# Optimization experiments

Measured on AMD Instinct MI355X. Metric: run time of the kernel, lower is better.

The kernel has to match this reference:

```python
import jax, jax.numpy as jnp
import numpy as np
from jax import lax


def T_grid(t, num_coeff):
    # Chebyshev polynomials T_0..T_{N-1} evaluated at t -> (N, len(t))
    rows = [jnp.ones_like(t), t]
    for _ in range(2, num_coeff):
        rows.append(2.0 * t * rows[-1] - rows[-2])
    return jnp.stack(rows[:num_coeff], axis=0)


def setup_inputs() -> dict:
    key = jax.random.key(0)
    k1, k2, k3, k4, k5 = jax.random.split(key, 5)
    B, D, H, N, T = 128, 512, 1024, 32, 16
    return {
        "t_span": jnp.linspace(0.0, 1.0, T, dtype=jnp.float32),
        "y_init": jax.random.normal(k1, (B, D), dtype=jnp.float32),
        "B_init": jax.random.uniform(k2, (B, D, N), dtype=jnp.float32),
        "W1": jax.random.normal(k3, (D, H), dtype=jnp.float32) / jnp.sqrt(jnp.float32(D)),
        "b1": jax.random.normal(k4, (H,), dtype=jnp.float32),
        "W2": jax.random.normal(k5, (H, D), dtype=jnp.float32) / jnp.sqrt(jnp.float32(H)),
        "num_coeff_per_dim": 32,
        "max_iters": 10,
    }


def reference(t_span, y_init, B_init, W1, b1, W2, num_coeff_per_dim, max_iters):
    N = num_coeff_per_dim
    t0, t1 = t_span[0], t_span[-1]

    # Chebyshev-Gauss-Lobatto nodes on [-1, 1] and Simpson midpoints interleaved
    t_cheb = -jnp.cos(jnp.pi * (jnp.arange(N, dtype=t_span.dtype) / (N - 1)))  # (N,)
    mids = 0.5 * (t_cheb[1:] + t_cheb[:-1])
    t_simpsons = jnp.zeros(2 * N - 1, dtype=t_span.dtype).at[::2].set(t_cheb).at[1::2].set(mids)
    t_true = t0 + 0.5 * (t1 - t0) * (t_simpsons + 1.0)  # (2N-1,)

    Phi_f = T_grid(t_simpsons, N)        # (N, 2N-1)
    Phi = Phi_f[:, ::2]                  # (N, N), invert ONCE (reused every iter)
    Phi_inv = jnp.linalg.inv(Phi)
    widths = (t_true[2::2] - t_true[:-2:2]) / 6.0  # (N-1,) Simpson interval weights

    def f_all(Y):  # vector field f(t, y) = tanh(y @ W1 + t*b1) @ W2, all nodes at once
        # Y: (B, D, M) with M = 2N-1
        h = jnp.tanh(jnp.einsum("bdm,dh->bhm", Y, W1) + t_true[None, None, :] * b1[None, :, None])
        return jnp.einsum("bhm,hd->bdm", h, W2)

    def step(Bc, _):
        approx = jnp.einsum("bdn,nm->bdm", Bc, Phi_f)          # (B, D, 2N-1)
        fap = f_all(approx)
        # Simpson's rule per Chebyshev interval, then cumulative integral S
        s = widths * (fap[..., :-2:2] + 4.0 * fap[..., 1:-1:2] + fap[..., 2::2])  # (B,D,N-1)
        S = jnp.concatenate([jnp.zeros_like(s[..., :1]), jnp.cumsum(s, axis=-1)], axis=-1)
        # torch.linalg.solve(Phi, S + y0, left=False): Bn @ Phi = S + y0
        Bn = (S + y_init[..., None]) @ Phi_inv
        return Bn, None

    B_final, _ = lax.scan(step, B_init, None, length=max_iters)

    t_out = -1.0 + 2.0 * (t_span - t0) / (t1 - t0)
    Phi_out = T_grid(t_out, N)                                  # (N, T)
    approx = jnp.einsum("bdn,nt->bdt", B_final, Phi_out)        # (B, D, T)
    return jnp.moveaxis(approx, -1, 0), B_final                 # (T, B, D), (B, D, N)
```

## Files before the change

### kernel.cpp

```cpp
#include <hip/hip_runtime.h>
#include <hip/hip_bf16.h>
#include <math.h>

#define BB 128
#define DD 512
#define HH 1024
#define NB 32
#define MM 63
#define TT 16
#define ITERS 10

#define OFF_U       0
#define OFF_TTRUE   64
#define OFF_PHIOUT  128
#define OFF_PHIF_BF 1024
#define OFF_QT_BF   2048
#define HDRF        4096
#define OFF_PTPA    HDRF
#define OFF_PTP0    (OFF_PTPA + 2097152)
#define OFF_W1P     (OFF_PTP0 + 2097152)
#define OFF_W2P     (OFF_W1P + 262144)
#define OFF_WWP     (OFF_W2P + 262144)
#define OFF_YW1     (OFF_WWP + 524288)

typedef __attribute__((ext_vector_type(8))) short bf16x8;
typedef __attribute__((ext_vector_type(4))) float f32x4;

static __device__ __forceinline__ unsigned short f2bf(float f) {
    unsigned int x = __builtin_bit_cast(unsigned int, f);
    unsigned int r = x + 0x7FFFu + ((x >> 16) & 1u);
    return (unsigned short)(r >> 16);
}

static __device__ __forceinline__ void store4bf(unsigned short* p,
                                                float v0, float v1, float v2, float v3) {
    unsigned int lo = (unsigned int)f2bf(v0) | ((unsigned int)f2bf(v1) << 16);
    unsigned int hi = (unsigned int)f2bf(v2) | ((unsigned int)f2bf(v3) << 16);
    uint2 u; u.x = lo; u.y = hi;
    *(uint2*)p = u;
}

static __device__ __forceinline__ float tanh_fast(float x) {
    float e = exp2f(x * 2.88539008177793f);
    return 1.0f - 2.0f / (e + 1.0f);
}

static __device__ __forceinline__ unsigned short* aS(unsigned short* smA, int r, int c16) {
    return (unsigned short*)((char*)smA + (((r << 10) + (c16 << 4)) ^ ((r & 7) << 4)));
}

__global__ __launch_bounds__(256) void prologue_kernel(
        const float* __restrict__ t_span, const float* __restrict__ W1,
        const float* __restrict__ W2, const float* __restrict__ y_init,
        float* __restrict__ ws) {
    __shared__ __align__(16) char smem[66560];
    const int bid  = blockIdx.x;
    const int t    = threadIdx.x;
    const int lane = t & 63;
    const int w    = t >> 6;
    const int q    = lane >> 4;
    const int l15  = lane & 15;

    if (bid == 0) {
        double* tsim    = (double*)(smem + 0);
        double* ttrue_d = (double*)(smem + 512);
        double* wid     = (double*)(smem + 1024);
        double* phid    = (double*)(smem + 1280);
        double* aug     = (double*)(smem + 17408);
        double* mlt     = (double*)(smem + 33792);
        double* Rl      = (double*)(smem + 34048);
        double* Qd      = (double*)(smem + 50176);
        int*    piv_s   = (int*)(smem + 66304);

        const int rgrp = t >> 6;
        const double PI = 3.14159265358979323846;
        const double t0 = (double)t_span[0];
        const double t1 = (double)t_span[TT - 1];

        if (t < MM) {
            double v;
            if ((t & 1) == 0) {
                int j = t >> 1;
                v = -cos(PI * (double)j / (double)(NB - 1));
            } else {
                int i = t >> 1;
                double a = -cos(PI * (double)i / (double)(NB - 1));
                double b = -cos(PI * (double)(i + 1) / (double)(NB - 1));
                v = 0.5 * (a + b);
            }
            tsim[t] = v;
            ttrue_d[t] = t0 + 0.5 * (t1 - t0) * (v + 1.0);
        }
        __syncthreads();
        if (t < 31) wid[t] = (ttrue_d[2 * t + 2] - ttrue_d[2 * t]) / 6.0;
        if (t < MM) ws[OFF_TTRUE + t] = (float)ttrue_d[t];
        if (t == 63) ws[OFF_TTRUE + 63] = 0.0f;

        if (t < MM) {
            double x = tsim[t];
            double r0 = 1.0, r1 = x;
            phid[0 * MM + t] = r0;
            phid[1 * MM + t] = r1;
            for (int n = 2; n < NB; n++) {
                double r2 = 2.0 * x * r1 - r0;
                phid[n * MM + t] = r2;
                r0 = r1; r1 = r2;
            }
        }
        __syncthreads();

        {
            unsigned short* pf = (unsigned short*)(ws + OFF_PHIF_BF);
            for (int f = t; f < 64 * 32; f += 256) {
                int m = f >> 5, n = f & 31;
                pf[f] = f2bf(m < MM ? (float)phid[n * MM + m] : 0.0f);
            }
        }

        for (int f = t; f < NB * 64; f += 256) {
            int r = f >> 6, c = f & 63;
            double v;
            if (c < NB) v = phid[r * MM + 2 * c];
            else        v = ((c - NB) == r) ? 1.0 : 0.0;
            aug[f] = v;
        }
        __syncthreads();

        for (int k = 0; k < NB; k++) {
            if (t < 32) {
                double v = (t >= k) ? fabs(aug[t * 64 + k]) : -1.0;
                int idx = t;
                #pragma unroll
                for (int off = 16; off >= 1; off >>= 1) {
                    double ov = __shfl_xor(v, off);
                    int    oi = __shfl_xor(idx, off);
                    if (ov > v) { v = ov; idx = oi; }
                }
                if (t == 0) *piv_s = idx;
            }
            __syncthreads();
            const int p = *piv_s;
            if (t < 64) {
                double pv   = aug[p * 64 + k];
                double rowp = aug[p * 64 + t];
                double rowk = aug[k * 64 + t];
                aug[k * 64 + t] = rowp / pv;
                if (p != k) aug[p * 64 + t] = rowk;
            }
            __syncthreads();
            if (t < 32) mlt[t] = (t == k) ? 0.0 : aug[t * 64 + k];
            __syncthreads();
            {
                double pk = aug[k * 64 + lane];
                #pragma unroll
                for (int i = 0; i < 8; i++) {
                    int r = rgrp * 8 + i;
                    aug[r * 64 + lane] -= mlt[r] * pk;
                }
            }
            __syncthreads();
        }

        if (t < MM) {
            double acc = 0.0;
            Rl[t * NB + 0] = 0.0;
            for (int i = 1; i < NB; i++) {
                int ip = i - 1;
                double wv = 0.0;
                if (t == 2 * ip)     wv += wid[ip];
                if (t == 2 * ip + 1) wv += 4.0 * wid[ip];
                if (t == 2 * ip + 2) wv += wid[ip];
                acc += wv;
                Rl[t * NB + i] = acc;
            }
        }
        __syncthreads();

        for (int f = t; f < MM * NB; f += 256) {
            int m = f >> 5, j = f & 31;
            double s = 0.0;
            for (int i = 0; i < NB; i++) s += Rl[m * NB + i] * aug[i * 64 + 32 + j];
            Qd[f] = s;
        }
        __syncthreads();

        {
            unsigned short* qt = (unsigned short*)(ws + OFF_QT_BF);
            for (int f = t; f < 32 * 64; f += 256) {
                int j = f >> 6, m = f & 63;
                qt[f] = f2bf(m < MM ? (float)Qd[m * NB + j] : 0.0f);
            }
        }
        if (t < NB) {
            double s = 0.0;
            for (int i = 0; i < NB; i++) s += aug[i * 64 + 32 + t];
            ws[OFF_U + t] = (float)s;
        }
        if (t < TT) {
            double x = -1.0 + 2.0 * ((double)t_span[t] - t0) / (t1 - t0);
            double r0 = 1.0, r1 = x;
            ws[OFF_PHIOUT + 0 * TT + t] = 1.0f;
            ws[OFF_PHIOUT + 1 * TT + t] = (float)x;
            for (int n = 2; n < NB; n++) {
                double r2 = 2.0 * x * r1 - r0;
                ws[OFF_PHIOUT + n * TT + t] = (float)r2;
                r0 = r1; r1 = r2;
            }
        }
        return;
    }

    if (bid <= 64) {
        unsigned short* W1p = (unsigned short*)(ws + OFF_W1P);
        const int hb = bid - 1;
        #pragma unroll
        for (int i = 0; i < 4; i++) {
            int f = i * 256 + t;
            int ds = f >> 6, ln = f & 63;
            int qq = ln >> 4, ll = ln & 15;
            unsigned short tmp[8];
            #pragma unroll
            for (int e = 0; e < 8; e++)
                tmp[e] = f2bf(W1[(size_t)(ds * 32 + qq * 8 + e) * HH + hb * 16 + ll]);
            *(uint4*)(W1p + ((size_t)(hb * 16 + ds) * 64 + ln) * 8) = *(uint4*)tmp;
        }
        return;
    }

    if (bid <= 96) {
        unsigned short* W2p = (unsigned short*)(ws + OFF_W2P);
        const int db = bid - 65;
        #pragma unroll
        for (int i = 0; i < 8; i++) {
            int f = i * 256 + t;
            int hs = f >> 6, ln = f & 63;
            int qq = ln >> 4, ll = ln & 15;
            unsigned short tmp[8];
            #pragma unroll
            for (int e = 0; e < 8; e++)
                tmp[e] = f2bf(W2[(size_t)(hs * 32 + qq * 8 + e) * DD + db * 16 + ll]);
            *(uint4*)(W2p + ((size_t)(db * 32 + hs) * 64 + ln) * 8) = *(uint4*)tmp;
        }
        return;
    }

    if (bid <= 352) {
        unsigned short* WWp = (unsigned short*)(ws + OFF_WWP);
        unsigned short* pbounce = (unsigned short*)smem;
        const int idx   = bid - 97;
        const int h2blk = idx & 7;
        const int hpb   = idx >> 3;
        const int h2w   = h2blk * 128 + w * 32;

        f32x4 acc[2][2] = {};
        #pragma unroll 4
        for (int ds = 0; ds < 16; ds++) {
            bf16x8 a[2];
            #pragma unroll
            for (int mt = 0; mt < 2; mt++) {
                const float* w2r = W2 + (size_t)(hpb * 32 + mt * 16 + l15) * DD + ds * 32 + q * 8;
                float4 va = *(const float4*)w2r;
                float4 vb = *(const float4*)(w2r + 4);
                unsigned short tmp[8] = { f2bf(va.x), f2bf(va.y), f2bf(va.z), f2bf(va.w),
                                          f2bf(vb.x), f2bf(vb.y), f2bf(vb.z), f2bf(vb.w) };
                a[mt] = *(bf16x8*)tmp;
            }
            bf16x8 bb0, bb1;
            {
                unsigned short tb[8];
                #pragma unroll
                for (int e = 0; e < 8; e++)
                    tb[e] = f2bf(W1[(size_t)(ds * 32 + q * 8 + e) * HH + h2w + l15]);
                bb0 = *(bf16x8*)tb;
                #pragma unroll
                for (int e = 0; e < 8; e++)
                    tb[e] = f2bf(W1[(size_t)(ds * 32 + q * 8 + e) * HH + h2w + 16 + l15]);
                bb1 = *(bf16x8*)tb;
            }
            acc[0][0] = __builtin_amdgcn_mfma_f32_16x16x32_bf16(a[0], bb0, acc[0][0], 0, 0, 0);
            acc[0][1] = __builtin_amdgcn_mfma_f32_16x16x32_bf16(a[0], bb1, acc[0][1], 0, 0, 0);
            acc[1][0] = __builtin_amdgcn_mfma_f32_16x16x32_bf16(a[1], bb0, acc[1][0], 0, 0, 0);
            acc[1][1] = __builtin_amdgcn_mfma_f32_16x16x32_bf16(a[1], bb1, acc[1][1], 0, 0, 0);
        }
        unsigned short* pb = pbounce + w * 1024;
        #pragma unroll
        for (int mt = 0; mt < 2; mt++)
            #pragma unroll
            for (int nt = 0; nt < 2; nt++) {
                int lane8 = (mt * 2 + (q >> 1)) * 16 + l15;
                #pragma unroll
                for (int r = 0; r < 4; r++)
                    pb[(nt * 64 + lane8) * 8 + (q & 1) * 4 + r] = f2bf(acc[mt][nt][r]);
            }
        uint4 f0 = *(uint4*)(pb + (0 * 64 + lane) * 8);
        uint4 f1 = *(uint4*)(pb + (1 * 64 + lane) * 8);
        int h2b0 = h2w >> 4;
        *(uint4*)(WWp + ((size_t)(h2b0 + 0) * 32 + hpb) * 512 + lane * 8) = f0;
        *(uint4*)(WWp + ((size_t)(h2b0 + 1) * 32 + hpb) * 512 + lane * 8) = f1;
        return;
    }

    {
        float* yW1 = ws + OFF_YW1;
        const int idx   = bid - 353;
        const int h2blk = idx & 7;
        const int bblk  = idx >> 3;
        const int h2w   = h2blk * 128 + w * 32;

        f32x4 acc[2][2] = {};
        #pragma unroll 4
        for (int ds = 0; ds < 16; ds++) {
            bf16x8 a[2];
            #pragma unroll
            for (int mt = 0; mt < 2; mt++) {
                const float* yr = y_init + (size_t)(bblk * 32 + mt * 16 + l15) * DD + ds * 32 + q * 8;
                float4 va = *(const float4*)yr;
                float4 vb = *(const float4*)(yr + 4);
                unsigned short tmp[8] = { f2bf(va.x), f2bf(va.y), f2bf(va.z), f2bf(va.w),
                                          f2bf(vb.x), f2bf(vb.y), f2bf(vb.z), f2bf(vb.w) };
                a[mt] = *(bf16x8*)tmp;
            }
            bf16x8 bb0, bb1;
            {
                unsigned short tb[8];
                #pragma unroll
                for (int e = 0; e < 8; e++)
                    tb[e] = f2bf(W1[(size_t)(ds * 32 + q * 8 + e) * HH + h2w + l15]);
                bb0 = *(bf16x8*)tb;
                #pragma unroll
                for (int e = 0; e < 8; e++)
                    tb[e] = f2bf(W1[(size_t)(ds * 32 + q * 8 + e) * HH + h2w + 16 + l15]);
                bb1 = *(bf16x8*)tb;
            }
            acc[0][0] = __builtin_amdgcn_mfma_f32_16x16x32_bf16(a[0], bb0, acc[0][0], 0, 0, 0);
            acc[0][1] = __builtin_amdgcn_mfma_f32_16x16x32_bf16(a[0], bb1, acc[0][1], 0, 0, 0);
            acc[1][0] = __builtin_amdgcn_mfma_f32_16x16x32_bf16(a[1], bb0, acc[1][0], 0, 0, 0);
            acc[1][1] = __builtin_amdgcn_mfma_f32_16x16x32_bf16(a[1], bb1, acc[1][1], 0, 0, 0);
        }
        #pragma unroll
        for (int mt = 0; mt < 2; mt++)
            #pragma unroll
            for (int nt = 0; nt < 2; nt++)
                #pragma unroll
                for (int r = 0; r < 4; r++) {
                    int b  = bblk * 32 + mt * 16 + q * 4 + r;
                    int h2 = h2w + nt * 16 + l15;
                    yW1[(size_t)b * HH + h2] = acc[mt][nt][r];
                }
    }
}

__global__ __launch_bounds__(256) void k1_kernel(
        const float* __restrict__ B_init,
        const unsigned short* __restrict__ W1p,
        const float* __restrict__ b1,
        const float* __restrict__ ws,
        unsigned short* __restrict__ Ptp)
{
    __shared__ __align__(16) char smem[40960];
    unsigned short* smA  = (unsigned short*)smem;
    unsigned short* t_sb = (unsigned short*)smem;
    unsigned short* g_sb = (unsigned short*)(smem + 32768);

    const int t    = threadIdx.x;
    const int lane = t & 63;
    const int w    = t >> 6;
    const int q    = lane >> 4;
    const int l15  = lane & 15;
    const int b    = blockIdx.y;
    const int hblk = blockIdx.x;
    const int hw   = hblk * 128 + w * 32;

    {
        const float* Bi = B_init + (size_t)b * DD * NB;
        #pragma unroll 8
        for (int i = 0; i < 64; i++) {
            int f = i * 256 + t;
            int d = f >> 5, n = f & 31;
            *(unsigned short*)(smem + (((n << 10) + (d << 1)) ^ ((n & 7) << 4)))
                = f2bf(Bi[f]);
        }
    }
    __syncthreads();

    f32x4 acc[2][2] = {};
    const unsigned short* W1b = W1p + (size_t)(hw >> 4) * 8192;
    #pragma unroll 4
    for (int d0 = 0; d0 < DD; d0 += 32) {
        int c16 = (d0 >> 3) + q;
        int ds  = d0 >> 5;
        bf16x8 a0  = *(const bf16x8*)aS(smA, l15, c16);
        bf16x8 a1  = *(const bf16x8*)aS(smA, 16 + l15, c16);
        bf16x8 bb0 = *(const bf16x8*)(W1b + ds * 512 + lane * 8);
        bf16x8 bb1 = *(const bf16x8*)(W1b + 8192 + ds * 512 + lane * 8);
        acc[0][0] = __builtin_amdgcn_mfma_f32_16x16x32_bf16(a0, bb0, acc[0][0], 0, 0, 0);
        acc[0][1] = __builtin_amdgcn_mfma_f32_16x16x32_bf16(a0, bb1, acc[0][1], 0, 0, 0);
        acc[1][0] = __builtin_amdgcn_mfma_f32_16x16x32_bf16(a1, bb0, acc[1][0], 0, 0, 0);
        acc[1][1] = __builtin_amdgcn_mfma_f32_16x16x32_bf16(a1, bb1, acc[1][1], 0, 0, 0);
    }
    #pragma unroll
    for (int mt = 0; mt < 2; mt++)
        #pragma unroll
        for (int nt = 0; nt < 2; nt++) {
            int hl = w * 32 + nt * 16 + l15;
            store4bf(&g_sb[hl * 32 + mt * 16 + q * 4],
                     acc[mt][nt][0], acc[mt][nt][1], acc[mt][nt][2], acc[mt][nt][3]);
        }
    __syncthreads();

    f32x4 zacc[4][2] = {};
    const unsigned short* PF = (const unsigned short*)(ws + OFF_PHIF_BF);
    bf16x8 gb[2];
    #pragma unroll
    for (int nt = 0; nt < 2; nt++)
        gb[nt] = *(const bf16x8*)(&g_sb[(w * 32 + nt * 16 + l15) * 32 + q * 8]);
    #pragma unroll
    for (int mt = 0; mt < 4; mt++) {
        bf16x8 af = *(const bf16x8*)(PF + (mt * 16 + l15) * 32 + q * 8);
        zacc[mt][0] = __builtin_amdgcn_mfma_f32_16x16x32_bf16(af, gb[0], zacc[mt][0], 0, 0, 0);
        zacc[mt][1] = __builtin_amdgcn_mfma_f32_16x16x32_bf16(af, gb[1], zacc[mt][1], 0, 0, 0);
    }

    const float* TTp = ws + OFF_TTRUE;
    float b1v[2] = { b1[hw + l15], b1[hw + 16 + l15] };
    #pragma unroll
    for (int mt = 0; mt < 4; mt++) {
        float4 ttv = *(const float4*)(TTp + mt * 16 + q * 4);
        #pragma unroll
        for (int nt = 0; nt < 2; nt++) {
            int hl = w * 32 + nt * 16 + l15;
            float v0 = tanh_fast(zacc[mt][nt][0] + ttv.x * b1v[nt]);
            float v1 = tanh_fast(zacc[mt][nt][1] + ttv.y * b1v[nt]);
            float v2 = tanh_fast(zacc[mt][nt][2] + ttv.z * b1v[nt]);
            float v3 = tanh_fast(zacc[mt][nt][3] + ttv.w * b1v[nt]);
            store4bf(&t_sb[hl * 72 + mt * 16 + q * 4], v0, v1, v2, v3);
        }
    }
    __syncthreads();

    f32x4 pacc[2][2] = {};
    const unsigned short* QT = (const unsigned short*)(ws + OFF_QT_BF);
    #pragma unroll
    for (int ks = 0; ks < 2; ks++) {
        bf16x8 bt[2];
        #pragma unroll
        for (int nt = 0; nt < 2; nt++)
            bt[nt] = *(const bf16x8*)(&t_sb[(w * 32 + nt * 16 + l15) * 72 + ks * 32 + q * 8]);
        #pragma unroll
        for (int jt = 0; jt < 2; jt++) {
            bf16x8 aq = *(const bf16x8*)(QT + (jt * 16 + l15) * 64 + ks * 32 + q * 8);
            pacc[jt][0] = __builtin_amdgcn_mfma_f32_16x16x32_bf16(aq, bt[0], pacc[jt][0], 0, 0, 0);
            pacc[jt][1] = __builtin_amdgcn_mfma_f32_16x16x32_bf16(aq, bt[1], pacc[jt][1], 0, 0, 0);
        }
    }

    {
        unsigned short* pb = g_sb + w * 1024;
        #pragma unroll
        for (int jt = 0; jt < 2; jt++)
            #pragma unroll
            for (int nt = 0; nt < 2; nt++) {
                int grp = (nt * 2 + (l15 >> 3)) & 3;
                #pragma unroll
                for (int r = 0; r < 4; r++) {
                    int lane8 = grp * 16 + q * 4 + r;
                    pb[(jt * 64 + lane8) * 8 + (l15 & 7)] = f2bf(pacc[jt][nt][r]);
                }
            }
        int hs = hblk * 4 + w;
        uint4 f0 = *(uint4*)(pb + (0 * 64 + lane) * 8);
        uint4 f1 = *(uint4*)(pb + (1 * 64 + lane) * 8);
        *(uint4*)(Ptp + (((size_t)(b * 32 + hs) * 2 + 0) * 64 + lane) * 8) = f0;
        *(uint4*)(Ptp + (((size_t)(b * 32 + hs) * 2 + 1) * 64 + lane) * 8) = f1;
    }
}

__global__ __launch_bounds__(256) void kf_kernel(
        const unsigned short* __restrict__ Ptin,
        const unsigned short* __restrict__ WWp,
        const float* __restrict__ yW1,
        const float* __restrict__ b1,
        const float* __restrict__ ws,
        unsigned short* __restrict__ Ptout)
{
    __shared__ __align__(16) unsigned short t_sb[128 * 72];
    __shared__ __align__(16) unsigned short g_sb[128 * 32];

    const int t    = threadIdx.x;
    const int lane = t & 63;
    const int w    = t >> 6;
    const int q    = lane >> 4;
    const int l15  = lane & 15;
    const int b    = blockIdx.y;
    const int hblk = blockIdx.x;
    const int hw   = hblk * 128 + w * 32;

    f32x4 acc[2][2] = {};
    const unsigned short* Ab  = Ptin + (size_t)b * 32768;
    const unsigned short* WWb = WWp + (size_t)(hw >> 4) * 16384;
    #pragma unroll 4
    for (int s = 0; s < 32; s++) {
        bf16x8 a0  = *(const bf16x8*)(Ab + (s * 2 + 0) * 512 + lane * 8);
        bf16x8 a1  = *(const bf16x8*)(Ab + (s * 2 + 1) * 512 + lane * 8);
        bf16x8 bb0 = *(const bf16x8*)(WWb + s * 512 + lane * 8);
        bf16x8 bb1 = *(const bf16x8*)(WWb + 16384 + s * 512 + lane * 8);
        acc[0][0] = __builtin_amdgcn_mfma_f32_16x16x32_bf16(a0, bb0, acc[0][0], 0, 0, 0);
        acc[0][1] = __builtin_amdgcn_mfma_f32_16x16x32_bf16(a0, bb1, acc[0][1], 0, 0, 0);
        acc[1][0] = __builtin_amdgcn_mfma_f32_16x16x32_bf16(a1, bb0, acc[1][0], 0, 0, 0);
        acc[1][1] = __builtin_amdgcn_mfma_f32_16x16x32_bf16(a1, bb1, acc[1][1], 0, 0, 0);
    }

    const float* U = ws + OFF_U;
    float yw[2] = { yW1[(size_t)b * HH + hw + l15],
                    yW1[(size_t)b * HH + hw + 16 + l15] };
    #pragma unroll
    for (int mt = 0; mt < 2; mt++) {
        float4 uv = *(const float4*)(U + mt * 16 + q * 4);
        #pragma unroll
        for (int nt = 0; nt < 2; nt++) {
            int hl = w * 32 + nt * 16 + l15;
            store4bf(&g_sb[hl * 32 + mt * 16 + q * 4],
                     acc[mt][nt][0] + uv.x * yw[nt],
                     acc[mt][nt][1] + uv.y * yw[nt],
                     acc[mt][nt][2] + uv.z * yw[nt],
                     acc[mt][nt][3] + uv.w * yw[nt]);
        }
    }

    f32x4 zacc[4][2] = {};
    const unsigned short* PF = (const unsigned short*)(ws + OFF_PHIF_BF);
    bf16x8 gb[2];
    #pragma unroll
    for (int nt = 0; nt < 2; nt++)
        gb[nt] = *(const bf16x8*)(&g_sb[(w * 32 + nt * 16 + l15) * 32 + q * 8]);
    #pragma unroll
    for (int mt = 0; mt < 4; mt++) {
        bf16x8 af = *(const bf16x8*)(PF + (mt * 16 + l15) * 32 + q * 8);
        zacc[mt][0] = __builtin_amdgcn_mfma_f32_16x16x32_bf16(af, gb[0], zacc[mt][0], 0, 0, 0);
        zacc[mt][1] = __builtin_amdgcn_mfma_f32_16x16x32_bf16(af, gb[1], zacc[mt][1], 0, 0, 0);
    }

    const float* TTp = ws + OFF_TTRUE;
    float b1v[2] = { b1[hw + l15], b1[hw + 16 + l15] };
    #pragma unroll
    for (int mt = 0; mt < 4; mt++) {
        float4 ttv = *(const float4*)(TTp + mt * 16 + q * 4);
        #pragma unroll
        for (int nt = 0; nt < 2; nt++) {
            int hl = w * 32 + nt * 16 + l15;
            float v0 = tanh_fast(zacc[mt][nt][0] + ttv.x * b1v[nt]);
            float v1 = tanh_fast(zacc[mt][nt][1] + ttv.y * b1v[nt]);
            float v2 = tanh_fast(zacc[mt][nt][2] + ttv.z * b1v[nt]);
            float v3 = tanh_fast(zacc[mt][nt][3] + ttv.w * b1v[nt]);
            store4bf(&t_sb[hl * 72 + mt * 16 + q * 4], v0, v1, v2, v3);
        }
    }

    f32x4 pacc[2][2] = {};
    const unsigned short* QT = (const unsigned short*)(ws + OFF_QT_BF);
    #pragma unroll
    for (int ks = 0; ks < 2; ks++) {
        bf16x8 bt[2];
        #pragma unroll
        for (int nt = 0; nt < 2; nt++)
            bt[nt] = *(const bf16x8*)(&t_sb[(w * 32 + nt * 16 + l15) * 72 + ks * 32 + q * 8]);
        #pragma unroll
        for (int jt = 0; jt < 2; jt++) {
            bf16x8 aq = *(const bf16x8*)(QT + (jt * 16 + l15) * 64 + ks * 32 + q * 8);
            pacc[jt][0] = __builtin_amdgcn_mfma_f32_16x16x32_bf16(aq, bt[0], pacc[jt][0], 0, 0, 0);
            pacc[jt][1] = __builtin_amdgcn_mfma_f32_16x16x32_bf16(aq, bt[1], pacc[jt][1], 0, 0, 0);
        }
    }

    {
        unsigned short* pb = g_sb + w * 1024;
        #pragma unroll
        for (int jt = 0; jt < 2; jt++)
            #pragma unroll
            for (int nt = 0; nt < 2; nt++) {
                int grp = (nt * 2 + (l15 >> 3)) & 3;
                #pragma unroll
                for (int r = 0; r < 4; r++) {
                    int lane8 = grp * 16 + q * 4 + r;
                    pb[(jt * 64 + lane8) * 8 + (l15 & 7)] = f2bf(pacc[jt][nt][r]);
                }
            }
        int hs = hblk * 4 + w;
        uint4 f0 = *(uint4*)(pb + (0 * 64 + lane) * 8);
        uint4 f1 = *(uint4*)(pb + (1 * 64 + lane) * 8);
        *(uint4*)(Ptout + (((size_t)(b * 32 + hs) * 2 + 0) * 64 + lane) * 8) = f0;
        *(uint4*)(Ptout + (((size_t)(b * 32 + hs) * 2 + 1) * 64 + lane) * 8) = f1;
    }
}

__global__ __launch_bounds__(256) void k2f_kernel(
        const unsigned short* __restrict__ Ptp,
        const unsigned short* __restrict__ W2p,
        const float* __restrict__ y_init,
        const float* __restrict__ ws,
        float* __restrict__ out)
{
    __shared__ __align__(16) float ls[4 * 544];
    __shared__ float phiout_s[NB * TT];

    const int t    = threadIdx.x;
    const int lane = t & 63;
    const int w    = t >> 6;
    const int q    = lane >> 4;
    const int l15  = lane & 15;
    const int b    = blockIdx.y;
    const int dblk = blockIdx.x;
    const int dw   = dblk * 64 + w * 16;

    for (int f = t; f < NB * TT; f += 256) phiout_s[f] = ws[OFF_PHIOUT + f];

    f32x4 acc[2] = {};
    const unsigned short* Ab  = Ptp + (size_t)b * 32768;
    const unsigned short* W2b = W2p + (size_t)(dblk * 4 + w) * 16384;
    #pragma unroll 4
    for (int s = 0; s < 32; s++) {
        bf16x8 a0 = *(const bf16x8*)(Ab + (s * 2 + 0) * 512 + lane * 8);
        bf16x8 a1 = *(const bf16x8*)(Ab + (s * 2 + 1) * 512 + lane * 8);
        bf16x8 bb = *(const bf16x8*)(W2b + s * 512 + lane * 8);
        acc[0] = __builtin_amdgcn_mfma_f32_16x16x32_bf16(a0, bb, acc[0], 0, 0, 0);
        acc[1] = __builtin_amdgcn_mfma_f32_16x16x32_bf16(a1, bb, acc[1], 0, 0, 0);
    }

    const float* U = ws + OFF_U;
    float yv = y_init[(size_t)b * DD + dw + l15];
    #pragma unroll
    for (int mt = 0; mt < 2; mt++) {
        float4 uv = *(const float4*)(U + mt * 16 + q * 4);
        #pragma unroll
        for (int r = 0; r < 4; r++) {
            int j = mt * 16 + q * 4 + r;
            float uvr = (r == 0) ? uv.x : (r == 1) ? uv.y : (r == 2) ? uv.z : uv.w;
            ls[w * 544 + j * 17 + l15] = acc[mt][r] + yv * uvr;
        }
    }
    __syncthreads();

    float* out1 = out + (size_t)TT * BB * DD;
    #pragma unroll
    for (int it = 0; it < 8; it++) {
        int f = it * 64 + lane;
        int d_l = f >> 5, j2 = f & 31;
        out1[((size_t)b * DD + dw + d_l) * NB + j2] = ls[w * 544 + j2 * 17 + d_l];
    }

    #pragma unroll
    for (int i = 0; i < 4; i++) {
        int idx = i * 256 + t;
        int t16 = idx >> 6, dl = idx & 63;
        float s = 0.f;
        #pragma unroll
        for (int n = 0; n < NB; n++)
            s += ls[(dl >> 4) * 544 + n * 17 + (dl & 15)] * phiout_s[n * TT + t16];
        out[(size_t)t16 * (BB * DD) + (size_t)b * DD + dblk * 64 + dl] = s;
    }
}

extern "C" void kernel_launch(void* const* d_in, const int* in_sizes, int n_in,
                              void* d_out, int out_size, void* d_ws, size_t ws_size,
                              hipStream_t stream) {
    const float* t_span = (const float*)d_in[0];
    const float* y_init = (const float*)d_in[1];
    const float* B_init = (const float*)d_in[2];
    const float* W1     = (const float*)d_in[3];
    const float* b1     = (const float*)d_in[4];
    const float* W2     = (const float*)d_in[5];
    float* ws  = (float*)d_ws;
    float* out = (float*)d_out;

    unsigned short* W1p  = (unsigned short*)(ws + OFF_W1P);
    unsigned short* W2p  = (unsigned short*)(ws + OFF_W2P);
    unsigned short* WWp  = (unsigned short*)(ws + OFF_WWP);
    float*          yW1  = ws + OFF_YW1;
    unsigned short* PtpA = (unsigned short*)(ws + OFF_PTPA);
    unsigned short* PtpB = (unsigned short*)(ws + OFF_PTP0);

    prologue_kernel<<<dim3(385), 256, 0, stream>>>(t_span, W1, W2, y_init, ws);

    k1_kernel<<<dim3(8, BB), 256, 0, stream>>>(B_init, W1p, b1, ws, PtpA);

    unsigned short* pin  = PtpA;
    unsigned short* pout = PtpB;
    for (int it = 1; it < ITERS; it++) {
        kf_kernel<<<dim3(8, BB), 256, 0, stream>>>(pin, WWp, yW1, b1, ws, pout);
        unsigned short* tmp = pin; pin = pout; pout = tmp;
    }
    k2f_kernel<<<dim3(8, BB), 256, 0, stream>>>(pin, W2p, y_init, ws, out);
}
```

Measured before the change: 389.9 us.

## Stage W1 column slab in LDS for prologue GEMMs and reorder block-to-tile mapping

In the prologue's WW and yW1 GEMM blocks, a 512x32 slab of W1 is now converted to bf16 once into shared memory, and each warp reads it from there. Previously every lane gathered strided fp32 W1 elements from global memory on each k-step. Work is repartitioned so the four warps of a block share the same h2 columns. The main kernels switch from a 2D grid to a 1D grid with batch as the fastest index, so concurrently running blocks share the same weight tiles and get better L2 reuse. The cost is an extra LDS fill and a barrier per prologue block. The yW1 part now launches only 32 blocks, each covering all 128 batch rows.

```diff
diff --git a/kernel.cpp b/kernel.cpp
--- a/kernel.cpp
+++ b/kernel.cpp
@@ -244,13 +244,22 @@
         return;
     }
 
+    unsigned short* lw1 = (unsigned short*)smem;
+
     if (bid <= 352) {
         unsigned short* WWp = (unsigned short*)(ws + OFF_WWP);
-        unsigned short* pbounce = (unsigned short*)smem;
+        unsigned short* pbounce = (unsigned short*)(smem + 36864);
         const int idx   = bid - 97;
-        const int h2blk = idx & 7;
-        const int hpb   = idx >> 3;
-        const int h2w   = h2blk * 128 + w * 32;
+        const int h2grp = idx & 31;
+        const int hpb   = (idx >> 5) * 4 + w;
+        const int h2c0  = h2grp * 32;
+
+        for (int i = 0; i < 64; i++) {
+            int f = i * 256 + t;
+            int row = f >> 5, col = f & 31;
+            lw1[row * 36 + col] = f2bf(W1[(size_t)row * HH + h2c0 + col]);
+        }
+        __syncthreads();
 
         f32x4 acc[2][2] = {};
         #pragma unroll 4
@@ -270,11 +279,11 @@
                 unsigned short tb[8];
                 #pragma unroll
                 for (int e = 0; e < 8; e++)
-                    tb[e] = f2bf(W1[(size_t)(ds * 32 + q * 8 + e) * HH + h2w + l15]);
+                    tb[e] = lw1[(ds * 32 + q * 8 + e) * 36 + l15];
                 bb0 = *(bf16x8*)tb;
                 #pragma unroll
                 for (int e = 0; e < 8; e++)
-                    tb[e] = f2bf(W1[(size_t)(ds * 32 + q * 8 + e) * HH + h2w + 16 + l15]);
+                    tb[e] = lw1[(ds * 32 + q * 8 + e) * 36 + 16 + l15];
                 bb1 = *(bf16x8*)tb;
             }
             acc[0][0] = __builtin_amdgcn_mfma_f32_16x16x32_bf16(a[0], bb0, acc[0][0], 0, 0, 0);
@@ -294,7 +303,7 @@
             }
         uint4 f0 = *(uint4*)(pb + (0 * 64 + lane) * 8);
         uint4 f1 = *(uint4*)(pb + (1 * 64 + lane) * 8);
-        int h2b0 = h2w >> 4;
+        int h2b0 = h2grp * 2;
         *(uint4*)(WWp + ((size_t)(h2b0 + 0) * 32 + hpb) * 512 + lane * 8) = f0;
         *(uint4*)(WWp + ((size_t)(h2b0 + 1) * 32 + hpb) * 512 + lane * 8) = f1;
         return;
@@ -302,10 +311,15 @@
 
     {
         float* yW1 = ws + OFF_YW1;
-        const int idx   = bid - 353;
-        const int h2blk = idx & 7;
-        const int bblk  = idx >> 3;
-        const int h2w   = h2blk * 128 + w * 32;
+        const int h2grp = bid - 353;
+        const int h2c0  = h2grp * 32;
+
+        for (int i = 0; i < 64; i++) {
+            int f = i * 256 + t;
+            int row = f >> 5, col = f & 31;
+            lw1[row * 36 + col] = f2bf(W1[(size_t)row * HH + h2c0 + col]);
+        }
+        __syncthreads();
 
         f32x4 acc[2][2] = {};
         #pragma unroll 4
@@ -313,7 +327,7 @@
             bf16x8 a[2];
             #pragma unroll
             for (int mt = 0; mt < 2; mt++) {
-                const float* yr = y_init + (size_t)(bblk * 32 + mt * 16 + l15) * DD + ds * 32 + q * 8;
+                const float* yr = y_init + (size_t)(w * 32 + mt * 16 + l15) * DD + ds * 32 + q * 8;
                 float4 va = *(const float4*)yr;
                 float4 vb = *(const float4*)(yr + 4);
                 unsigned short tmp[8] = { f2bf(va.x), f2bf(va.y), f2bf(va.z), f2bf(va.w),
@@ -325,11 +339,11 @@
                 unsigned short tb[8];
                 #pragma unroll
                 for (int e = 0; e < 8; e++)
-                    tb[e] = f2bf(W1[(size_t)(ds * 32 + q * 8 + e) * HH + h2w + l15]);
+                    tb[e] = lw1[(ds * 32 + q * 8 + e) * 36 + l15];
                 bb0 = *(bf16x8*)tb;
                 #pragma unroll
                 for (int e = 0; e < 8; e++)
-                    tb[e] = f2bf(W1[(size_t)(ds * 32 + q * 8 + e) * HH + h2w + 16 + l15]);
+                    tb[e] = lw1[(ds * 32 + q * 8 + e) * 36 + 16 + l15];
                 bb1 = *(bf16x8*)tb;
             }
             acc[0][0] = __builtin_amdgcn_mfma_f32_16x16x32_bf16(a[0], bb0, acc[0][0], 0, 0, 0);
@@ -343,8 +357,8 @@
             for (int nt = 0; nt < 2; nt++)
                 #pragma unroll
                 for (int r = 0; r < 4; r++) {
-                    int b  = bblk * 32 + mt * 16 + q * 4 + r;
-                    int h2 = h2w + nt * 16 + l15;
+                    int b  = w * 32 + mt * 16 + q * 4 + r;
+                    int h2 = h2c0 + nt * 16 + l15;
                     yW1[(size_t)b * HH + h2] = acc[mt][nt][r];
                 }
     }
@@ -367,8 +381,9 @@
     const int w    = t >> 6;
     const int q    = lane >> 4;
     const int l15  = lane & 15;
-    const int b    = blockIdx.y;
-    const int hblk = blockIdx.x;
+    const int bid  = blockIdx.x;
+    const int b    = bid & 127;
+    const int hblk = bid >> 7;
     const int hw   = hblk * 128 + w * 32;
 
     {
@@ -491,8 +506,9 @@
     const int w    = t >> 6;
     const int q    = lane >> 4;
     const int l15  = lane & 15;
-    const int b    = blockIdx.y;
-    const int hblk = blockIdx.x;
+    const int bid  = blockIdx.x;
+    const int b    = bid & 127;
+    const int hblk = bid >> 7;
     const int hw   = hblk * 128 + w * 32;
 
     f32x4 acc[2][2] = {};
@@ -608,8 +624,9 @@
     const int w    = t >> 6;
     const int q    = lane >> 4;
     const int l15  = lane & 15;
-    const int b    = blockIdx.y;
-    const int dblk = blockIdx.x;
+    const int bid  = blockIdx.x;
+    const int b    = bid & 127;
+    const int dblk = bid >> 7;
     const int dw   = dblk * 64 + w * 16;
 
     for (int f = t; f < NB * TT; f += 256) phiout_s[f] = ws[OFF_PHIOUT + f];
@@ -681,13 +698,13 @@
 
     prologue_kernel<<<dim3(385), 256, 0, stream>>>(t_span, W1, W2, y_init, ws);
 
-    k1_kernel<<<dim3(8, BB), 256, 0, stream>>>(B_init, W1p, b1, ws, PtpA);
+    k1_kernel<<<dim3(1024), 256, 0, stream>>>(B_init, W1p, b1, ws, PtpA);
 
     unsigned short* pin  = PtpA;
     unsigned short* pout = PtpB;
     for (int it = 1; it < ITERS; it++) {
-        kf_kernel<<<dim3(8, BB), 256, 0, stream>>>(pin, WWp, yW1, b1, ws, pout);
+        kf_kernel<<<dim3(1024), 256, 0, stream>>>(pin, WWp, yW1, b1, ws, pout);
         unsigned short* tmp = pin; pin = pout; pout = tmp;
     }
-    k2f_kernel<<<dim3(8, BB), 256, 0, stream>>>(pin, W2p, y_init, ws, out);
-}
+    k2f_kernel<<<dim3(1024), 256, 0, stream>>>(pin, W2p, y_init, ws, out);
+}
```

New measurement: 368.5 us. -5.5%, faster.
